# Kernel optimization log

Measured on AMD Instinct MI355X. Metric: run time of the kernel, lower is better.

## Reference

```python
import jax, jax.numpy as jnp
import numpy as np

CHUNK = 32
EPS = 1e-6

def _l2norm(x):
    return x * jax.lax.rsqrt(jnp.sum(x * x, axis=-1, keepdims=True) + EPS)

def setup_inputs() -> dict:
    key = jax.random.key(0)
    k1, k2, k3, k4 = jax.random.split(key, 4)
    b, h, L, dk, dv = 4, 8, 4096, 128, 128
    return {
        'q': jax.random.normal(k1, (b, h, L, dk), dtype=jnp.float32),
        'k': jax.random.normal(k2, (b, h, L, dk), dtype=jnp.float32),
        'v': jax.random.normal(k3, (b, h, L, dv), dtype=jnp.float32),
        'beta': jax.random.uniform(k4, (b, h, L), dtype=jnp.float32),
    }

def _delta_rule_chunkwise(q, k, v, beta):
    b, h, L, dk = q.shape
    dv = v.shape[-1]
    c = CHUNK
    assert L % c == 0, 'L must be a multiple of chunk_size (no padding path)'
    n = L // c

    q = _l2norm(q)
    k = _l2norm(k)
    v = v * beta[..., None]
    k_beta = k * beta[..., None]

    # [b,h,n,c,d]
    resh = lambda t: t.reshape(b, h, n, c, t.shape[-1])
    qc, kc, vc, kbc = resh(q), resh(k), resh(v), resh(k_beta)

    ones = jnp.ones((c, c), dtype=jnp.float32)
    strict_lower = jnp.tril(ones, -1)      # below diagonal
    lower_inc = jnp.tril(ones, 0)          # diagonal and below

    # inv = -(k_beta @ k^T) with upper-incl-diag zeroed, then forward substitution
    inv = -jnp.einsum('bhncd,bhned->bhnce', kbc, kc) * strict_lower
    for i in range(1, c):
        # inv[..., i, :i] += inv[..., i, :] @ inv[..., :, :i]
        upd = jnp.einsum('bhnk,bhnkj->bhnj', inv[..., i, :], inv[..., :, :i])
        inv = inv.at[..., i, :i].add(upd)
    inv = inv + jnp.eye(c, dtype=inv.dtype)

    u = jnp.einsum('bhnce,bhned->bhncd', inv, vc)    # [b,h,n,c,dv]
    w = jnp.einsum('bhnce,bhned->bhncd', inv, kbc)   # [b,h,n,c,dk]

    # scan over chunks carrying state S [b,h,dk,dv]
    def step(S, inp):
        q_i, k_i, u0_i, w_i = inp  # [b,h,c,d*]
        attn = jnp.einsum('bhcd,bhed->bhce', q_i, k_i) * lower_inc
        u_i = u0_i - jnp.einsum('bhcd,bhdv->bhcv', w_i, S)
        out_i = jnp.einsum('bhcd,bhdv->bhcv', q_i, S) + jnp.einsum('bhce,bhev->bhcv', attn, u_i)
        S = S + jnp.einsum('bhcd,bhcv->bhdv', k_i, u_i)
        return S, out_i

    chunk_first = lambda t: jnp.moveaxis(t, 2, 0)  # [n,b,h,c,d]
    S0 = jnp.zeros((b, h, dk, dv), dtype=q.dtype)
    S, out = jax.lax.scan(step, S0, (chunk_first(qc), chunk_first(kc), chunk_first(u), chunk_first(w)))
    out = jnp.moveaxis(out, 0, 2).reshape(b, h, L, dv)
    return out, S

def reference(q, k, v, beta):
    out, S = _delta_rule_chunkwise(q, k, v, beta)
    return out
```

## Files before the change

### kernel.cpp

```cpp
#include <hip/hip_runtime.h>
#include <math.h>

#define CHUNK 32
#define DK 128
#define DV 128
#define L_SEQ 4096
#define BH 32
#define NCH 128

typedef __attribute__((ext_vector_type(8))) short bf16x8;
typedef __attribute__((ext_vector_type(4))) float f32x4;

union U8 { unsigned int u[4]; bf16x8 v; };

#define MFMA16(a, b, c) __builtin_amdgcn_mfma_f32_16x16x32_bf16((a), (b), (c), 0, 0, 0)
#define LGKM_WAIT() __asm__ __volatile__("s_waitcnt lgkmcnt(0)" ::: "memory")

__device__ __forceinline__ unsigned short f2bf(float x){
    unsigned int u = __builtin_bit_cast(unsigned int, x);
    u = u + 0x7FFFu + ((u >> 16) & 1u);
    return (unsigned short)(u >> 16);
}
__device__ __forceinline__ unsigned int pk2(float a, float b){
    unsigned int r;
    asm("v_cvt_pk_bf16_f32 %0, %1, %2" : "=v"(r) : "v"(a), "v"(b));
    return r;
}

__device__ __forceinline__ bf16x8 afragF32(const float (*M)[36], int row, int q8){
    float4 f0 = *(const float4*)&M[row][q8];
    float4 f1 = *(const float4*)&M[row][q8 + 4];
    U8 t;
    t.u[0] = pk2(f0.x, f0.y); t.u[1] = pk2(f0.z, f0.w);
    t.u[2] = pk2(f1.x, f1.y); t.u[3] = pk2(f1.z, f1.w);
    return t.v;
}
__device__ __forceinline__ bf16x8 bfragF32(const float (*M)[36], int q8, int col){
    U8 t;
#pragma unroll
    for (int j2 = 0; j2 < 4; ++j2)
        t.u[j2] = pk2(M[q8 + 2*j2][col], M[q8 + 2*j2 + 1][col]);
    return t.v;
}


__global__ __launch_bounds__(64, 1)
void prep_kernel(const float* __restrict__ q, const float* __restrict__ k,
                 const float* __restrict__ beta,
                 unsigned short* __restrict__ qw, unsigned short* __restrict__ kw,
                 unsigned short* __restrict__ Tw, unsigned short* __restrict__ Aw)
{
    const int bc = blockIdx.x;
    const size_t row0 = (size_t)bc * CHUNK;
    const int l = threadIdx.x;
    const int r = l & 31, h = l >> 5;
    const int quad = (l >> 4) & 3, ln15 = l & 15, q8 = quad * 8;

    __shared__ unsigned short qn_s[32][136], kn_s[32][136], kb_s[32][136];
    __shared__ float Ms[32][36];
    __shared__ float Rs[32][36];

    const float bet = beta[row0 + r];

    {
        const float4* gp = (const float4*)(q + (row0 + r) * DK + 64 * h);
        float vb[64]; float s = 0.f;
#pragma unroll
        for (int e = 0; e < 16; ++e){
            float4 a = gp[e];
            vb[4*e+0]=a.x; vb[4*e+1]=a.y; vb[4*e+2]=a.z; vb[4*e+3]=a.w;
            s += a.x*a.x + a.y*a.y + a.z*a.z + a.w*a.w;
        }
        s += __shfl_xor(s, 32);
        float sc = rsqrtf(s + 1e-6f);
#pragma unroll
        for (int e = 0; e < 8; ++e){
            U8 t;
#pragma unroll
            for (int j = 0; j < 4; ++j)
                t.u[j] = pk2(vb[8*e+2*j] * sc, vb[8*e+2*j+1] * sc);
            *(bf16x8*)&qn_s[r][64*h + 8*e] = t.v;
            *(bf16x8*)(qw + (row0 + r) * DK + 64*h + 8*e) = t.v;
        }
    }
    {
        const float4* gp = (const float4*)(k + (row0 + r) * DK + 64 * h);
        float vb[64]; float s = 0.f;
#pragma unroll
        for (int e = 0; e < 16; ++e){
            float4 a = gp[e];
            vb[4*e+0]=a.x; vb[4*e+1]=a.y; vb[4*e+2]=a.z; vb[4*e+3]=a.w;
            s += a.x*a.x + a.y*a.y + a.z*a.z + a.w*a.w;
        }
        s += __shfl_xor(s, 32);
        float sc = rsqrtf(s + 1e-6f);
#pragma unroll
        for (int e = 0; e < 8; ++e){
            U8 t, tb;
#pragma unroll
            for (int j = 0; j < 4; ++j){
                float x0 = vb[8*e+2*j] * sc, x1 = vb[8*e+2*j+1] * sc;
                t.u[j]  = pk2(x0, x1);
                tb.u[j] = pk2(x0 * bet, x1 * bet);
            }
            *(bf16x8*)&kn_s[r][64*h + 8*e] = t.v;
            *(bf16x8*)&kb_s[r][64*h + 8*e] = tb.v;
            *(bf16x8*)(kw + (row0 + r) * DK + 64*h + 8*e) = t.v;
        }
    }
    LGKM_WAIT();

    f32x4 Z = {0.f, 0.f, 0.f, 0.f};
    f32x4 Bacc[2][2] = {{Z, Z}, {Z, Z}};
    f32x4 Aacc[2][2] = {{Z, Z}, {Z, Z}};
#pragma unroll
    for (int ks = 0; ks < 4; ++ks){
        bf16x8 bF[2];
        bF[0] = *(const bf16x8*)&kn_s[ln15][32*ks + q8];
        bF[1] = *(const bf16x8*)&kn_s[16 + ln15][32*ks + q8];
#pragma unroll
        for (int mt = 0; mt < 2; ++mt){
            bf16x8 aK = *(const bf16x8*)&kb_s[16*mt + ln15][32*ks + q8];
            bf16x8 aQ = *(const bf16x8*)&qn_s[16*mt + ln15][32*ks + q8];
#pragma unroll
            for (int nt = 0; nt < 2; ++nt){
                Bacc[mt][nt] = MFMA16(aK, bF[nt], Bacc[mt][nt]);
                Aacc[mt][nt] = MFMA16(aQ, bF[nt], Aacc[mt][nt]);
            }
        }
    }

    f32x4 Rc[2][2];
#pragma unroll
    for (int mt = 0; mt < 2; ++mt)
#pragma unroll
    for (int nt = 0; nt < 2; ++nt)
#pragma unroll
    for (int rg = 0; rg < 4; ++rg){
        int row = 16*mt + 4*quad + rg, col = 16*nt + ln15;
        float av = (col <= row) ? Aacc[mt][nt][rg] : 0.f;
        Aw[((size_t)bc << 10) + row*32 + col] = f2bf(av);
        float bm = (col < row) ? -Bacc[mt][nt][rg] : 0.f;
        Ms[row][col] = bm;
        Rc[mt][nt][rg] = bm + ((col == row) ? 1.f : 0.f);
    }

#pragma unroll 1
    for (int rd = 0; rd < 4; ++rd){
        LGKM_WAIT();
        bf16x8 Am[2], Bm2[2];
#pragma unroll
        for (int mt = 0; mt < 2; ++mt) Am[mt] = afragF32(Ms, 16*mt + ln15, q8);
#pragma unroll
        for (int nt = 0; nt < 2; ++nt) Bm2[nt] = bfragF32(Ms, q8, 16*nt + ln15);
        f32x4 Mq[2][2];
#pragma unroll
        for (int mt = 0; mt < 2; ++mt)
#pragma unroll
        for (int nt = 0; nt < 2; ++nt)
            Mq[mt][nt] = MFMA16(Am[mt], Bm2[nt], Z);
#pragma unroll
        for (int mt = 0; mt < 2; ++mt)
#pragma unroll
        for (int nt = 0; nt < 2; ++nt)
#pragma unroll
        for (int rg = 0; rg < 4; ++rg){
            int row = 16*mt + 4*quad + rg, col = 16*nt + ln15;
            Rs[row][col] = Rc[mt][nt][rg];
            Ms[row][col] = Mq[mt][nt][rg];
        }
        LGKM_WAIT();
        bf16x8 Ar[2], Bq[2];
#pragma unroll
        for (int mt = 0; mt < 2; ++mt) Ar[mt] = afragF32(Rs, 16*mt + ln15, q8);
#pragma unroll
        for (int nt = 0; nt < 2; ++nt) Bq[nt] = bfragF32(Ms, q8, 16*nt + ln15);
#pragma unroll
        for (int mt = 0; mt < 2; ++mt)
#pragma unroll
        for (int nt = 0; nt < 2; ++nt)
            Rc[mt][nt] = MFMA16(Ar[mt], Bq[nt], Rc[mt][nt]);
    }

#pragma unroll
    for (int mt = 0; mt < 2; ++mt)
#pragma unroll
    for (int nt = 0; nt < 2; ++nt)
#pragma unroll
    for (int rg = 0; rg < 4; ++rg){
        int row = 16*mt + 4*quad + rg, col = 16*nt + ln15;
        Tw[((size_t)bc << 10) + row*32 + col] = f2bf(Rc[mt][nt][rg]);
    }
}


__global__ __launch_bounds__(64, 1)
void scan_kernel(const float* __restrict__ v, const float* __restrict__ beta,
                 const unsigned short* __restrict__ qw, const unsigned short* __restrict__ kw,
                 const unsigned short* __restrict__ Tw, const unsigned short* __restrict__ Aw,
                 float* __restrict__ out)
{
    const int id = blockIdx.x;
    const int bh = id & 31, cb = id >> 5, c0 = cb * 16;
    const int l = threadIdx.x;
    const int quad = (l >> 4) & 3, ln15 = l & 15, q8 = quad * 8;
    const int hi = l >> 5;

    __shared__ unsigned short knR[4392];
    __shared__ unsigned short Xt[16][40];
    __shared__ unsigned short ut[16][40];

    const f32x4 Z = {0.f, 0.f, 0.f, 0.f};
    f32x4 Sacc[8];
#pragma unroll
    for (int t = 0; t < 8; ++t) Sacc[t] = Z;

    const size_t bhL = (size_t)bh * L_SEQ;
    const int a0 = (((l & 16) << 1) | ln15) << 2;
    const int a1 = a0 + 64;

    bf16x8 kAa[2][4], kAb[2][4];
    bf16x8 qA[2][4], tA[2], aA[2], knA[8], uB;
    float vr[8], br[8];

    auto loadK = [&](int ch, bf16x8 (&kA)[2][4]){
        const unsigned short* kp = kw + (bhL + (size_t)ch * CHUNK) * DK;
#pragma unroll
        for (int mt = 0; mt < 2; ++mt)
#pragma unroll
        for (int ks = 0; ks < 4; ++ks)
            kA[mt][ks] = *(const bf16x8*)(kp + (16*mt + ln15) * DK + 32*ks + q8);
    };
    auto loadQ = [&](int ch){
        const unsigned short* qp = qw + (bhL + (size_t)ch * CHUNK) * DK;
#pragma unroll
        for (int mt = 0; mt < 2; ++mt)
#pragma unroll
        for (int ks = 0; ks < 4; ++ks)
            qA[mt][ks] = *(const bf16x8*)(qp + (16*mt + ln15) * DK + 32*ks + q8);
    };
    auto loadT = [&](int ch){
        const unsigned short* Tp = Tw + ((size_t)(bh * NCH + ch) << 10);
#pragma unroll
        for (int mt = 0; mt < 2; ++mt)
            tA[mt] = *(const bf16x8*)(Tp + (16*mt + ln15) * 32 + q8);
    };
    auto loadA = [&](int ch){
        const unsigned short* Ap = Aw + ((size_t)(bh * NCH + ch) << 10);
#pragma unroll
        for (int mt = 0; mt < 2; ++mt)
            aA[mt] = *(const bf16x8*)(Ap + (16*mt + ln15) * 32 + q8);
    };
    auto loadVB = [&](int ch){
        const size_t row0 = bhL + (size_t)ch * CHUNK;
#pragma unroll
        for (int g = 0; g < 8; ++g){
            int i = 16*(g >> 2) + 4*quad + (g & 3);
            vr[g] = v[(row0 + i) * DV + c0 + ln15];
            br[g] = beta[row0 + i];
        }
    };

    loadK(0, kAa);
    loadQ(0); loadT(0); loadA(0); loadVB(0);
    loadK(1, kAb);
    {
        U8 z; z.u[0] = 0u; z.u[1] = 0u; z.u[2] = 0u; z.u[3] = 0u;
        uB = z.v;
#pragma unroll
        for (int t = 0; t < 8; ++t) knA[t] = z.v;
    }

    auto body = [&](int ch, bf16x8 (&cur)[2][4]){
        const size_t row0 = bhL + (size_t)ch * CHUNK;

#pragma unroll
        for (int t = 0; t < 8; ++t)
            Sacc[t] = MFMA16(knA[t], uB, Sacc[t]);

        int P[8][2];
#pragma unroll
        for (int t = 0; t < 8; ++t){
            P[t][0] = (int)pk2(Sacc[t][0], Sacc[t][1]);
            P[t][1] = (int)pk2(Sacc[t][2], Sacc[t][3]);
        }
        bf16x8 SB[4];
#pragma unroll
        for (int ks = 0; ks < 4; ++ks){
            U8 sb;
            int e, f;
            e = __builtin_amdgcn_ds_bpermute(a0, P[2*ks][0]);
            f = __builtin_amdgcn_ds_bpermute(a0, P[2*ks+1][0]);
            sb.u[0] = (unsigned)(hi ? f : e);
            e = __builtin_amdgcn_ds_bpermute(a0, P[2*ks][1]);
            f = __builtin_amdgcn_ds_bpermute(a0, P[2*ks+1][1]);
            sb.u[1] = (unsigned)(hi ? f : e);
            e = __builtin_amdgcn_ds_bpermute(a1, P[2*ks][0]);
            f = __builtin_amdgcn_ds_bpermute(a1, P[2*ks+1][0]);
            sb.u[2] = (unsigned)(hi ? f : e);
            e = __builtin_amdgcn_ds_bpermute(a1, P[2*ks][1]);
            f = __builtin_amdgcn_ds_bpermute(a1, P[2*ks+1][1]);
            sb.u[3] = (unsigned)(hi ? f : e);
            SB[ks] = sb.v;
        }

        f32x4 Y[2] = {Z, Z}, Op[2] = {Z, Z};
#pragma unroll
        for (int ks = 0; ks < 4; ++ks)
#pragma unroll
        for (int mt = 0; mt < 2; ++mt){
            Y[mt]  = MFMA16(cur[mt][ks], SB[ks], Y[mt]);
            Op[mt] = MFMA16(qA[mt][ks],  SB[ks], Op[mt]);
        }

#pragma unroll
        for (int mt = 0; mt < 2; ++mt){
            unsigned int w0 = pk2(br[4*mt+0] * (vr[4*mt+0] - Y[mt][0]),
                                  br[4*mt+1] * (vr[4*mt+1] - Y[mt][1]));
            unsigned int w1 = pk2(br[4*mt+2] * (vr[4*mt+2] - Y[mt][2]),
                                  br[4*mt+3] * (vr[4*mt+3] - Y[mt][3]));
            *(unsigned int*)&Xt[ln15][16*mt + 4*quad]     = w0;
            *(unsigned int*)&Xt[ln15][16*mt + 4*quad + 2] = w1;
        }

#pragma unroll
        for (int mt = 0; mt < 2; ++mt)
#pragma unroll
        for (int ks = 0; ks < 4; ++ks){
            int i = 16*mt + ln15;
            int ad = i * 136 + (i >> 3) * 16 + 32*ks + q8;
            *(bf16x8*)&knR[ad] = cur[mt][ks];
        }

        bf16x8 Xb = *(const bf16x8*)&Xt[ln15][q8];

        unsigned int rja[32];
#pragma unroll
        for (int t = 0; t < 4; ++t)
#pragma unroll
        for (int j = 0; j < 8; ++j)
            rja[8*t + j] = knR[(q8 + j) * 136 + ((q8 + j) >> 3) * 16 + 16*t + ln15];

        f32x4 U[2];
#pragma unroll
        for (int mt = 0; mt < 2; ++mt) U[mt] = MFMA16(tA[mt], Xb, Z);

#pragma unroll
        for (int mt = 0; mt < 2; ++mt){
            *(unsigned int*)&ut[ln15][16*mt + 4*quad]     = pk2(U[mt][0], U[mt][1]);
            *(unsigned int*)&ut[ln15][16*mt + 4*quad + 2] = pk2(U[mt][2], U[mt][3]);
        }

#pragma unroll
        for (int t = 0; t < 4; ++t){
            U8 kk;
            kk.u[0] = rja[8*t+0] | (rja[8*t+1] << 16);
            kk.u[1] = rja[8*t+2] | (rja[8*t+3] << 16);
            kk.u[2] = rja[8*t+4] | (rja[8*t+5] << 16);
            kk.u[3] = rja[8*t+6] | (rja[8*t+7] << 16);
            knA[t] = kk.v;
        }

        uB = *(const bf16x8*)&ut[ln15][q8];

        const int chn = (ch + 1 < NCH) ? ch + 1 : NCH - 1;
        const int ch2 = (ch + 2 < NCH) ? ch + 2 : NCH - 1;
        loadQ(chn); loadT(chn); loadVB(chn);
        loadK(ch2, cur);

        unsigned int rjb[32];
#pragma unroll
        for (int t = 0; t < 4; ++t)
#pragma unroll
        for (int j = 0; j < 8; ++j)
            rjb[8*t + j] = knR[(q8 + j) * 136 + ((q8 + j) >> 3) * 16 + 16*(t + 4) + ln15];

        f32x4 O[2];
#pragma unroll
        for (int mt = 0; mt < 2; ++mt) O[mt] = MFMA16(aA[mt], uB, Op[mt]);
#pragma unroll
        for (int mt = 0; mt < 2; ++mt)
#pragma unroll
        for (int rg = 0; rg < 4; ++rg)
            out[(row0 + 16*mt + 4*quad + rg) * DV + c0 + ln15] = O[mt][rg];

#pragma unroll
        for (int t = 0; t < 4; ++t){
            U8 kk;
            kk.u[0] = rjb[8*t+0] | (rjb[8*t+1] << 16);
            kk.u[1] = rjb[8*t+2] | (rjb[8*t+3] << 16);
            kk.u[2] = rjb[8*t+4] | (rjb[8*t+5] << 16);
            kk.u[3] = rjb[8*t+6] | (rjb[8*t+7] << 16);
            knA[t + 4] = kk.v;
        }
        loadA(chn);
    };

    for (int ch = 0; ch < NCH; ch += 2){
        body(ch,     kAa);
        body(ch + 1, kAb);
    }
}


__global__ __launch_bounds__(512, 1)
void deltanet_fused(const float* __restrict__ q, const float* __restrict__ k,
                    const float* __restrict__ v, const float* __restrict__ beta,
                    float* __restrict__ out)
{
    const int bh = blockIdx.x;
    const int tid = threadIdx.x;
    const int n = L_SEQ / CHUNK;

    __shared__ float S[DK][DV + 1];
    __shared__ float qs[CHUNK][DK + 1];
    __shared__ float ks[CHUNK][DK + 1];
    __shared__ float vs[CHUNK][DV + 1];
    __shared__ float kbs[CHUNK][DK + 1];
    __shared__ float T[CHUNK][CHUNK + 1];
    __shared__ float at[CHUNK][CHUNK + 1];
    __shared__ float bet[CHUNK];

    for (int idx = tid; idx < DK * DV; idx += 512)
        S[idx / DV][idx % DV] = 0.f;
    __syncthreads();

    const size_t base_bh = (size_t)bh * L_SEQ;

    for (int ch = 0; ch < n; ++ch){
        const size_t row0 = base_bh + (size_t)ch * CHUNK;
        for (int idx = tid; idx < CHUNK * DK; idx += 512){
            int r = idx >> 7, c = idx & 127;
            size_t g = (row0 + (size_t)r) * DK + c;
            qs[r][c] = q[g]; ks[r][c] = k[g]; vs[r][c] = v[g];
        }
        if (tid < CHUNK) bet[tid] = beta[row0 + tid];
        __syncthreads();
        if (tid < 64){
            int r = tid & 31;
            const float* src = (tid < 32) ? &qs[r][0] : &ks[r][0];
            float s = 0.f;
            for (int d = 0; d < DK; ++d){ float x = src[d]; s += x * x; }
            at[(tid < 32) ? 0 : 1][r] = 1.0f / sqrtf(s + 1e-6f);
        }
        __syncthreads();
        for (int idx = tid; idx < CHUNK * DK; idx += 512){
            int r = idx >> 7, c = idx & 127;
            float qq = qs[r][c] * at[0][r];
            float kk = ks[r][c] * at[1][r];
            float b = bet[r];
            qs[r][c] = qq; ks[r][c] = kk; kbs[r][c] = kk * b; vs[r][c] *= b;
        }
        __syncthreads();
        for (int idx = tid; idx < CHUNK * CHUNK; idx += 512){
            int i = idx >> 5, j = idx & 31;
            float s = 0.f;
            if (j < i){
                for (int d = 0; d < DK; ++d) s += kbs[i][d] * ks[j][d];
                s = -s;
            }
            T[i][j] = s;
        }
        __syncthreads();
        for (int i = 1; i < CHUNK; ++i){
            float upd = 0.f;
            if (tid < i){
                int j = tid;
                for (int kk = j + 1; kk < i; ++kk) upd += T[i][kk] * T[kk][j];
            }
            __syncthreads();
            if (tid < i) T[i][tid] += upd;
            __syncthreads();
        }
        if (tid < CHUNK) T[tid][tid] = 1.0f;
        __syncthreads();
        {
            int c = tid & 127;
            int i0 = (tid >> 7) * 8;
            float uacc[8], wacc[8];
#pragma unroll
            for (int r = 0; r < 8; ++r){ uacc[r] = 0.f; wacc[r] = 0.f; }
            for (int j = 0; j < CHUNK; ++j){
                float vvv = vs[j][c], kb = kbs[j][c];
#pragma unroll
                for (int r = 0; r < 8; ++r){
                    float tt = T[i0 + r][j];
                    uacc[r] += tt * vvv; wacc[r] += tt * kb;
                }
            }
            __syncthreads();
#pragma unroll
            for (int r = 0; r < 8; ++r){ vs[i0 + r][c] = uacc[r]; kbs[i0 + r][c] = wacc[r]; }
        }
        __syncthreads();
        for (int idx = tid; idx < CHUNK * CHUNK; idx += 512){
            int i = idx >> 5, j = idx & 31;
            float s = 0.f;
            if (j <= i) for (int d = 0; d < DK; ++d) s += qs[i][d] * ks[j][d];
            at[i][j] = s;
        }
        __syncthreads();
        {
            int c = tid & 127;
            int i0 = (tid >> 7) * 8;
            float acc[8];
#pragma unroll
            for (int r = 0; r < 8; ++r) acc[r] = 0.f;
            for (int d = 0; d < DK; ++d){
                float sv = S[d][c];
#pragma unroll
                for (int r = 0; r < 8; ++r) acc[r] += kbs[i0 + r][d] * sv;
            }
#pragma unroll
            for (int r = 0; r < 8; ++r) vs[i0 + r][c] -= acc[r];
        }
        __syncthreads();
        {
            int c = tid & 127;
            int i0 = (tid >> 7) * 8;
            float acc[8];
#pragma unroll
            for (int r = 0; r < 8; ++r) acc[r] = 0.f;
            for (int d = 0; d < DK; ++d){
                float sv = S[d][c];
#pragma unroll
                for (int r = 0; r < 8; ++r) acc[r] += qs[i0 + r][d] * sv;
            }
            for (int j = 0; j < CHUNK; ++j){
                float uv = vs[j][c];
#pragma unroll
                for (int r = 0; r < 8; ++r) acc[r] += at[i0 + r][j] * uv;
            }
#pragma unroll
            for (int r = 0; r < 8; ++r)
                out[(row0 + (size_t)(i0 + r)) * DV + c] = acc[r];
        }
        __syncthreads();
        {
            int c = tid & 127;
            int d0 = (tid >> 7) * 32;
            float acc[32];
#pragma unroll
            for (int r = 0; r < 32; ++r) acc[r] = 0.f;
            for (int i = 0; i < CHUNK; ++i){
                float uv = vs[i][c];
#pragma unroll
                for (int r = 0; r < 32; ++r) acc[r] += ks[i][d0 + r] * uv;
            }
#pragma unroll
            for (int r = 0; r < 32; ++r) S[d0 + r][c] += acc[r];
        }
        __syncthreads();
    }
}

extern "C" void kernel_launch(void* const* d_in, const int* in_sizes, int n_in,
                              void* d_out, int out_size, void* d_ws, size_t ws_size,
                              hipStream_t stream) {
    const float* q = (const float*)d_in[0];
    const float* k = (const float*)d_in[1];
    const float* v = (const float*)d_in[2];
    const float* beta = (const float*)d_in[3];
    float* out = (float*)d_out;

    const size_t QK = (size_t)BH * L_SEQ * DK;
    const size_t TA = (size_t)BH * NCH * 1024;
    const size_t need = (2 * QK + 2 * TA) * sizeof(unsigned short);

    if (ws_size >= need){
        unsigned short* qwp = (unsigned short*)d_ws;
        unsigned short* kwp = qwp + QK;
        unsigned short* Twp = kwp + QK;
        unsigned short* Awp = Twp + TA;
        prep_kernel<<<BH * NCH, 64, 0, stream>>>(q, k, beta, qwp, kwp, Twp, Awp);
        scan_kernel<<<BH * 8, 64, 0, stream>>>(v, beta, qwp, kwp, Twp, Awp, out);
    } else {
        deltanet_fused<<<BH, 512, 0, stream>>>(q, k, v, beta, out);
    }
}
```

Before: 368.9 us.

## Precompute transposed K in prep and use permlane swaps in scan loop

The prep kernel now loads q/k straight into MFMA fragment registers instead of staging them in LDS. It also writes a transposed bf16 copy of normalized k to a new workspace buffer. The scan kernel loads this transposed K directly rather than transposing it through LDS every chunk. It replaces LDS staging and ds_bpermute shuffles with permlane16/32 swap instructions, dispatched over runtime-detected lane-order variants, and splits the MFMA accumulation chains for more ILP. This removes LDS traffic and waits from the serial scan, at the cost of more workspace memory, extra global reads and writes, and a larger fallback condition on workspace size.

```diff
diff --git a/kernel.cpp b/kernel.cpp
--- a/kernel.cpp
+++ b/kernel.cpp
@@ -10,11 +10,18 @@
 
 typedef __attribute__((ext_vector_type(8))) short bf16x8;
 typedef __attribute__((ext_vector_type(4))) float f32x4;
+typedef unsigned int uint32x2 __attribute__((ext_vector_type(2)));
 
 union U8 { unsigned int u[4]; bf16x8 v; };
 
 #define MFMA16(a, b, c) __builtin_amdgcn_mfma_f32_16x16x32_bf16((a), (b), (c), 0, 0, 0)
 #define LGKM_WAIT() __asm__ __volatile__("s_waitcnt lgkmcnt(0)" ::: "memory")
+
+#if __has_builtin(__builtin_amdgcn_permlane16_swap) && __has_builtin(__builtin_amdgcn_permlane32_swap)
+#define HAVE_PERMSWAP 1
+#else
+#define HAVE_PERMSWAP 0
+#endif
 
 __device__ __forceinline__ unsigned short f2bf(float x){
     unsigned int u = __builtin_bit_cast(unsigned int, x);
@@ -44,92 +51,174 @@
 }
 
 
-__global__ __launch_bounds__(64, 1)
+#if HAVE_PERMSWAP
+template<bool O16, bool O32>
+__device__ __forceinline__ bf16x8 quadperm(unsigned p0, unsigned p1, unsigned p2, unsigned p3,
+                                           bool hB, bool eqHS)
+{
+    uint32x2 t0 = __builtin_amdgcn_permlane16_swap(p0, p0, false, false);
+    uint32x2 t1 = __builtin_amdgcn_permlane16_swap(p1, p1, false, false);
+    uint32x2 t2 = __builtin_amdgcn_permlane16_swap(p2, p2, false, false);
+    uint32x2 t3 = __builtin_amdgcn_permlane16_swap(p3, p3, false, false);
+    unsigned p0e = O16 ? t0.y : t0.x, p0o = O16 ? t0.x : t0.y;
+    unsigned p1e = O16 ? t1.y : t1.x, p1o = O16 ? t1.x : t1.y;
+    unsigned p2e = O16 ? t2.y : t2.x, p2o = O16 ? t2.x : t2.y;
+    unsigned p3e = O16 ? t3.y : t3.x, p3o = O16 ? t3.x : t3.y;
+
+    auto word = [&](unsigned ae, unsigned ce) -> unsigned {
+        unsigned L = hB ? ce : ae;
+        uint32x2 x = __builtin_amdgcn_permlane32_swap(O32 ? ce : ae, O32 ? ae : ce, false, false);
+        unsigned C = O32 ? (hB ? x.y : x.x) : (hB ? x.x : x.y);
+        return eqHS ? L : C;
+    };
+    U8 r;
+    r.u[0] = word(p0e, p2e);
+    r.u[1] = word(p1e, p3e);
+    r.u[2] = word(p0o, p2o);
+    r.u[3] = word(p1o, p3o);
+    return r.v;
+}
+#else
+template<bool O16, bool O32>
+__device__ __forceinline__ bf16x8 quadperm(unsigned p0, unsigned p1, unsigned p2, unsigned p3,
+                                           bool hB, bool eqHS)
+{
+    (void)eqHS;
+    const int l = threadIdx.x;
+    const int ln15 = l & 15;
+    const int a0 = (((l & 16) << 1) | ln15) << 2;
+    const int a1 = a0 + 64;
+    U8 r; int e, f;
+    e = __builtin_amdgcn_ds_bpermute(a0, (int)p0); f = __builtin_amdgcn_ds_bpermute(a0, (int)p2);
+    r.u[0] = (unsigned)(hB ? f : e);
+    e = __builtin_amdgcn_ds_bpermute(a0, (int)p1); f = __builtin_amdgcn_ds_bpermute(a0, (int)p3);
+    r.u[1] = (unsigned)(hB ? f : e);
+    e = __builtin_amdgcn_ds_bpermute(a1, (int)p0); f = __builtin_amdgcn_ds_bpermute(a1, (int)p2);
+    r.u[2] = (unsigned)(hB ? f : e);
+    e = __builtin_amdgcn_ds_bpermute(a1, (int)p1); f = __builtin_amdgcn_ds_bpermute(a1, (int)p3);
+    r.u[3] = (unsigned)(hB ? f : e);
+    return r.v;
+}
+#endif
+
+
+__global__ __launch_bounds__(64)
 void prep_kernel(const float* __restrict__ q, const float* __restrict__ k,
                  const float* __restrict__ beta,
                  unsigned short* __restrict__ qw, unsigned short* __restrict__ kw,
-                 unsigned short* __restrict__ Tw, unsigned short* __restrict__ Aw)
+                 unsigned short* __restrict__ Tw, unsigned short* __restrict__ Aw,
+                 unsigned short* __restrict__ kwT)
 {
     const int bc = blockIdx.x;
     const size_t row0 = (size_t)bc * CHUNK;
     const int l = threadIdx.x;
-    const int r = l & 31, h = l >> 5;
     const int quad = (l >> 4) & 3, ln15 = l & 15, q8 = quad * 8;
 
-    __shared__ unsigned short qn_s[32][136], kn_s[32][136], kb_s[32][136];
     __shared__ float Ms[32][36];
     __shared__ float Rs[32][36];
-
-    const float bet = beta[row0 + r];
-
+    __shared__ __align__(16) unsigned short knS[4392];
+
+    const float bet0 = beta[row0 + ln15];
+    const float bet1 = beta[row0 + 16 + ln15];
+
+    bf16x8 qF[2][4];
     {
-        const float4* gp = (const float4*)(q + (row0 + r) * DK + 64 * h);
-        float vb[64]; float s = 0.f;
-#pragma unroll
-        for (int e = 0; e < 16; ++e){
-            float4 a = gp[e];
-            vb[4*e+0]=a.x; vb[4*e+1]=a.y; vb[4*e+2]=a.z; vb[4*e+3]=a.w;
-            s += a.x*a.x + a.y*a.y + a.z*a.z + a.w*a.w;
-        }
-        s += __shfl_xor(s, 32);
-        float sc = rsqrtf(s + 1e-6f);
-#pragma unroll
-        for (int e = 0; e < 8; ++e){
-            U8 t;
-#pragma unroll
-            for (int j = 0; j < 4; ++j)
-                t.u[j] = pk2(vb[8*e+2*j] * sc, vb[8*e+2*j+1] * sc);
-            *(bf16x8*)&qn_s[r][64*h + 8*e] = t.v;
-            *(bf16x8*)(qw + (row0 + r) * DK + 64*h + 8*e) = t.v;
-        }
-    }
+        float4 raw[2][4][2];
+        float s0 = 0.f, s1 = 0.f;
+#pragma unroll
+        for (int mt = 0; mt < 2; ++mt)
+#pragma unroll
+        for (int ks = 0; ks < 4; ++ks){
+            const float* p = q + (row0 + 16*mt + ln15) * DK + 32*ks + q8;
+            raw[mt][ks][0] = *(const float4*)p;
+            raw[mt][ks][1] = *(const float4*)(p + 4);
+        }
+#pragma unroll
+        for (int ks = 0; ks < 4; ++ks)
+#pragma unroll
+        for (int h = 0; h < 2; ++h){
+            float4 a = raw[0][ks][h], b = raw[1][ks][h];
+            s0 += a.x*a.x + a.y*a.y + a.z*a.z + a.w*a.w;
+            s1 += b.x*b.x + b.y*b.y + b.z*b.z + b.w*b.w;
+        }
+        s0 += __shfl_xor(s0, 16); s0 += __shfl_xor(s0, 32);
+        s1 += __shfl_xor(s1, 16); s1 += __shfl_xor(s1, 32);
+        float sc0 = rsqrtf(s0 + 1e-6f), sc1 = rsqrtf(s1 + 1e-6f);
+#pragma unroll
+        for (int mt = 0; mt < 2; ++mt){
+            float sc = mt ? sc1 : sc0;
+#pragma unroll
+            for (int ks = 0; ks < 4; ++ks){
+                float4 a = raw[mt][ks][0], b = raw[mt][ks][1];
+                U8 t;
+                t.u[0] = pk2(a.x*sc, a.y*sc); t.u[1] = pk2(a.z*sc, a.w*sc);
+                t.u[2] = pk2(b.x*sc, b.y*sc); t.u[3] = pk2(b.z*sc, b.w*sc);
+                qF[mt][ks] = t.v;
+                *(bf16x8*)(qw + (row0 + 16*mt + ln15) * DK + 32*ks + q8) = t.v;
+            }
+        }
+    }
+    bf16x8 kF[2][4], kB[2][4];
     {
-        const float4* gp = (const float4*)(k + (row0 + r) * DK + 64 * h);
-        float vb[64]; float s = 0.f;
-#pragma unroll
-        for (int e = 0; e < 16; ++e){
-            float4 a = gp[e];
-            vb[4*e+0]=a.x; vb[4*e+1]=a.y; vb[4*e+2]=a.z; vb[4*e+3]=a.w;
-            s += a.x*a.x + a.y*a.y + a.z*a.z + a.w*a.w;
-        }
-        s += __shfl_xor(s, 32);
-        float sc = rsqrtf(s + 1e-6f);
-#pragma unroll
-        for (int e = 0; e < 8; ++e){
-            U8 t, tb;
-#pragma unroll
-            for (int j = 0; j < 4; ++j){
-                float x0 = vb[8*e+2*j] * sc, x1 = vb[8*e+2*j+1] * sc;
-                t.u[j]  = pk2(x0, x1);
-                tb.u[j] = pk2(x0 * bet, x1 * bet);
-            }
-            *(bf16x8*)&kn_s[r][64*h + 8*e] = t.v;
-            *(bf16x8*)&kb_s[r][64*h + 8*e] = tb.v;
-            *(bf16x8*)(kw + (row0 + r) * DK + 64*h + 8*e) = t.v;
-        }
-    }
-    LGKM_WAIT();
-
+        float4 raw[2][4][2];
+        float s0 = 0.f, s1 = 0.f;
+#pragma unroll
+        for (int mt = 0; mt < 2; ++mt)
+#pragma unroll
+        for (int ks = 0; ks < 4; ++ks){
+            const float* p = k + (row0 + 16*mt + ln15) * DK + 32*ks + q8;
+            raw[mt][ks][0] = *(const float4*)p;
+            raw[mt][ks][1] = *(const float4*)(p + 4);
+        }
+#pragma unroll
+        for (int ks = 0; ks < 4; ++ks)
+#pragma unroll
+        for (int h = 0; h < 2; ++h){
+            float4 a = raw[0][ks][h], b = raw[1][ks][h];
+            s0 += a.x*a.x + a.y*a.y + a.z*a.z + a.w*a.w;
+            s1 += b.x*b.x + b.y*b.y + b.z*b.z + b.w*b.w;
+        }
+        s0 += __shfl_xor(s0, 16); s0 += __shfl_xor(s0, 32);
+        s1 += __shfl_xor(s1, 16); s1 += __shfl_xor(s1, 32);
+        float sc0 = rsqrtf(s0 + 1e-6f), sc1 = rsqrtf(s1 + 1e-6f);
+#pragma unroll
+        for (int mt = 0; mt < 2; ++mt){
+            float sc = mt ? sc1 : sc0;
+            float bb = mt ? bet1 : bet0;
+#pragma unroll
+            for (int ks = 0; ks < 4; ++ks){
+                float4 a = raw[mt][ks][0], b = raw[mt][ks][1];
+                float x0=a.x*sc, x1=a.y*sc, x2=a.z*sc, x3=a.w*sc;
+                float x4=b.x*sc, x5=b.y*sc, x6=b.z*sc, x7=b.w*sc;
+                U8 t, tb;
+                t.u[0]=pk2(x0,x1); t.u[1]=pk2(x2,x3); t.u[2]=pk2(x4,x5); t.u[3]=pk2(x6,x7);
+                tb.u[0]=pk2(x0*bb,x1*bb); tb.u[1]=pk2(x2*bb,x3*bb);
+                tb.u[2]=pk2(x4*bb,x5*bb); tb.u[3]=pk2(x6*bb,x7*bb);
+                kF[mt][ks] = t.v; kB[mt][ks] = tb.v;
+                *(bf16x8*)(kw + (row0 + 16*mt + ln15) * DK + 32*ks + q8) = t.v;
+            }
+        }
+    }
+#pragma unroll
+    for (int mt = 0; mt < 2; ++mt)
+#pragma unroll
+    for (int ks = 0; ks < 4; ++ks){
+        int i = 16*mt + ln15;
+        int ad = i * 136 + (i >> 3) * 16 + 32*ks + q8;
+        *(bf16x8*)&knS[ad] = kF[mt][ks];
+    }
     f32x4 Z = {0.f, 0.f, 0.f, 0.f};
     f32x4 Bacc[2][2] = {{Z, Z}, {Z, Z}};
     f32x4 Aacc[2][2] = {{Z, Z}, {Z, Z}};
 #pragma unroll
-    for (int ks = 0; ks < 4; ++ks){
-        bf16x8 bF[2];
-        bF[0] = *(const bf16x8*)&kn_s[ln15][32*ks + q8];
-        bF[1] = *(const bf16x8*)&kn_s[16 + ln15][32*ks + q8];
-#pragma unroll
-        for (int mt = 0; mt < 2; ++mt){
-            bf16x8 aK = *(const bf16x8*)&kb_s[16*mt + ln15][32*ks + q8];
-            bf16x8 aQ = *(const bf16x8*)&qn_s[16*mt + ln15][32*ks + q8];
-#pragma unroll
-            for (int nt = 0; nt < 2; ++nt){
-                Bacc[mt][nt] = MFMA16(aK, bF[nt], Bacc[mt][nt]);
-                Aacc[mt][nt] = MFMA16(aQ, bF[nt], Aacc[mt][nt]);
-            }
-        }
-    }
-
+    for (int ks = 0; ks < 4; ++ks)
+#pragma unroll
+    for (int mt = 0; mt < 2; ++mt)
+#pragma unroll
+    for (int nt = 0; nt < 2; ++nt){
+        Bacc[mt][nt] = MFMA16(kB[mt][ks], kF[nt][ks], Bacc[mt][nt]);
+        Aacc[mt][nt] = MFMA16(qF[mt][ks], kF[nt][ks], Aacc[mt][nt]);
+    }
     f32x4 Rc[2][2];
 #pragma unroll
     for (int mt = 0; mt < 2; ++mt)
@@ -144,7 +233,22 @@
         Ms[row][col] = bm;
         Rc[mt][nt][rg] = bm + ((col == row) ? 1.f : 0.f);
     }
-
+    {
+        unsigned short* kT = kwT + ((size_t)bc << 12);
+#pragma unroll
+        for (int t = 0; t < 8; ++t){
+            unsigned short rj[8];
+#pragma unroll
+            for (int j = 0; j < 8; ++j)
+                rj[j] = knS[(q8 + j) * 136 + ((q8 + j) >> 3) * 16 + 16*t + ln15];
+            U8 kk;
+            kk.u[0] = (unsigned)rj[0] | ((unsigned)rj[1] << 16);
+            kk.u[1] = (unsigned)rj[2] | ((unsigned)rj[3] << 16);
+            kk.u[2] = (unsigned)rj[4] | ((unsigned)rj[5] << 16);
+            kk.u[3] = (unsigned)rj[6] | ((unsigned)rj[7] << 16);
+            *(bf16x8*)(kT + (16*t + ln15) * 32 + q8) = kk.v;
+        }
+    }
 #pragma unroll 1
     for (int rd = 0; rd < 4; ++rd){
         LGKM_WAIT();
@@ -181,7 +285,6 @@
         for (int nt = 0; nt < 2; ++nt)
             Rc[mt][nt] = MFMA16(Ar[mt], Bq[nt], Rc[mt][nt]);
     }
-
 #pragma unroll
     for (int mt = 0; mt < 2; ++mt)
 #pragma unroll
@@ -194,21 +297,19 @@
 }
 
 
-__global__ __launch_bounds__(64, 1)
-void scan_kernel(const float* __restrict__ v, const float* __restrict__ beta,
-                 const unsigned short* __restrict__ qw, const unsigned short* __restrict__ kw,
-                 const unsigned short* __restrict__ Tw, const unsigned short* __restrict__ Aw,
-                 float* __restrict__ out)
+template<bool O16, bool O32>
+__device__ __forceinline__
+void scan_loop(const float* __restrict__ v, const float* __restrict__ beta,
+               const unsigned short* __restrict__ qw, const unsigned short* __restrict__ kw,
+               const unsigned short* __restrict__ kwT, const unsigned short* __restrict__ Tw,
+               const unsigned short* __restrict__ Aw, float* __restrict__ out)
 {
     const int id = blockIdx.x;
     const int bh = id & 31, cb = id >> 5, c0 = cb * 16;
     const int l = threadIdx.x;
     const int quad = (l >> 4) & 3, ln15 = l & 15, q8 = quad * 8;
-    const int hi = l >> 5;
-
-    __shared__ unsigned short knR[4392];
-    __shared__ unsigned short Xt[16][40];
-    __shared__ unsigned short ut[16][40];
+    const bool hB = (l & 32) != 0;
+    const bool eqHS = (hB == ((l & 16) != 0));
 
     const f32x4 Z = {0.f, 0.f, 0.f, 0.f};
     f32x4 Sacc[8];
@@ -216,20 +317,17 @@
     for (int t = 0; t < 8; ++t) Sacc[t] = Z;
 
     const size_t bhL = (size_t)bh * L_SEQ;
-    const int a0 = (((l & 16) << 1) | ln15) << 2;
-    const int a1 = a0 + 64;
-
-    bf16x8 kAa[2][4], kAb[2][4];
-    bf16x8 qA[2][4], tA[2], aA[2], knA[8], uB;
+
+    bf16x8 cur[2][4], qA[2][4], knA[8], tA[2], aA[2], uB;
     float vr[8], br[8];
 
-    auto loadK = [&](int ch, bf16x8 (&kA)[2][4]){
+    auto loadK = [&](int ch){
         const unsigned short* kp = kw + (bhL + (size_t)ch * CHUNK) * DK;
 #pragma unroll
         for (int mt = 0; mt < 2; ++mt)
 #pragma unroll
         for (int ks = 0; ks < 4; ++ks)
-            kA[mt][ks] = *(const bf16x8*)(kp + (16*mt + ln15) * DK + 32*ks + q8);
+            cur[mt][ks] = *(const bf16x8*)(kp + (16*mt + ln15) * DK + 32*ks + q8);
     };
     auto loadQ = [&](int ch){
         const unsigned short* qp = qw + (bhL + (size_t)ch * CHUNK) * DK;
@@ -260,10 +358,14 @@
             br[g] = beta[row0 + i];
         }
     };
-
-    loadK(0, kAa);
-    loadQ(0); loadT(0); loadA(0); loadVB(0);
-    loadK(1, kAb);
+    auto loadKT = [&](int ch){
+        const unsigned short* p = kwT + ((size_t)(bh * NCH + ch) << 12);
+#pragma unroll
+        for (int t = 0; t < 8; ++t)
+            knA[t] = *(const bf16x8*)(p + (16*t + ln15) * 32 + q8);
+    };
+
+    loadK(0); loadQ(0); loadT(0); loadA(0); loadVB(0);
     {
         U8 z; z.u[0] = 0u; z.u[1] = 0u; z.u[2] = 0u; z.u[3] = 0u;
         uB = z.v;
@@ -271,135 +373,99 @@
         for (int t = 0; t < 8; ++t) knA[t] = z.v;
     }
 
-    auto body = [&](int ch, bf16x8 (&cur)[2][4]){
+    for (int ch = 0; ch < NCH; ++ch){
         const size_t row0 = bhL + (size_t)ch * CHUNK;
+        const int chn = (ch + 1 < NCH) ? ch + 1 : NCH - 1;
 
 #pragma unroll
         for (int t = 0; t < 8; ++t)
             Sacc[t] = MFMA16(knA[t], uB, Sacc[t]);
-
-        int P[8][2];
+        loadKT(ch);
+
+        unsigned P[8][2];
 #pragma unroll
         for (int t = 0; t < 8; ++t){
-            P[t][0] = (int)pk2(Sacc[t][0], Sacc[t][1]);
-            P[t][1] = (int)pk2(Sacc[t][2], Sacc[t][3]);
+            P[t][0] = pk2(Sacc[t][0], Sacc[t][1]);
+            P[t][1] = pk2(Sacc[t][2], Sacc[t][3]);
         }
         bf16x8 SB[4];
 #pragma unroll
-        for (int ks = 0; ks < 4; ++ks){
-            U8 sb;
-            int e, f;
-            e = __builtin_amdgcn_ds_bpermute(a0, P[2*ks][0]);
-            f = __builtin_amdgcn_ds_bpermute(a0, P[2*ks+1][0]);
-            sb.u[0] = (unsigned)(hi ? f : e);
-            e = __builtin_amdgcn_ds_bpermute(a0, P[2*ks][1]);
-            f = __builtin_amdgcn_ds_bpermute(a0, P[2*ks+1][1]);
-            sb.u[1] = (unsigned)(hi ? f : e);
-            e = __builtin_amdgcn_ds_bpermute(a1, P[2*ks][0]);
-            f = __builtin_amdgcn_ds_bpermute(a1, P[2*ks+1][0]);
-            sb.u[2] = (unsigned)(hi ? f : e);
-            e = __builtin_amdgcn_ds_bpermute(a1, P[2*ks][1]);
-            f = __builtin_amdgcn_ds_bpermute(a1, P[2*ks+1][1]);
-            sb.u[3] = (unsigned)(hi ? f : e);
-            SB[ks] = sb.v;
-        }
-
-        f32x4 Y[2] = {Z, Z}, Op[2] = {Z, Z};
-#pragma unroll
         for (int ks = 0; ks < 4; ++ks)
+            SB[ks] = quadperm<O16, O32>(P[2*ks][0], P[2*ks][1], P[2*ks+1][0], P[2*ks+1][1], hB, eqHS);
+
+        f32x4 Y0[2] = {Z, Z}, Y1[2] = {Z, Z}, Op0[2] = {Z, Z}, Op1[2] = {Z, Z};
 #pragma unroll
         for (int mt = 0; mt < 2; ++mt){
-            Y[mt]  = MFMA16(cur[mt][ks], SB[ks], Y[mt]);
-            Op[mt] = MFMA16(qA[mt][ks],  SB[ks], Op[mt]);
-        }
-
-#pragma unroll
-        for (int mt = 0; mt < 2; ++mt){
-            unsigned int w0 = pk2(br[4*mt+0] * (vr[4*mt+0] - Y[mt][0]),
-                                  br[4*mt+1] * (vr[4*mt+1] - Y[mt][1]));
-            unsigned int w1 = pk2(br[4*mt+2] * (vr[4*mt+2] - Y[mt][2]),
-                                  br[4*mt+3] * (vr[4*mt+3] - Y[mt][3]));
-            *(unsigned int*)&Xt[ln15][16*mt + 4*quad]     = w0;
-            *(unsigned int*)&Xt[ln15][16*mt + 4*quad + 2] = w1;
-        }
-
-#pragma unroll
-        for (int mt = 0; mt < 2; ++mt)
-#pragma unroll
-        for (int ks = 0; ks < 4; ++ks){
-            int i = 16*mt + ln15;
-            int ad = i * 136 + (i >> 3) * 16 + 32*ks + q8;
-            *(bf16x8*)&knR[ad] = cur[mt][ks];
-        }
-
-        bf16x8 Xb = *(const bf16x8*)&Xt[ln15][q8];
-
-        unsigned int rja[32];
-#pragma unroll
-        for (int t = 0; t < 4; ++t)
-#pragma unroll
-        for (int j = 0; j < 8; ++j)
-            rja[8*t + j] = knR[(q8 + j) * 136 + ((q8 + j) >> 3) * 16 + 16*t + ln15];
+            Y0[mt]  = MFMA16(cur[mt][0], SB[0], Y0[mt]);
+            Y0[mt]  = MFMA16(cur[mt][1], SB[1], Y0[mt]);
+            Y1[mt]  = MFMA16(cur[mt][2], SB[2], Y1[mt]);
+            Y1[mt]  = MFMA16(cur[mt][3], SB[3], Y1[mt]);
+            Op0[mt] = MFMA16(qA[mt][0],  SB[0], Op0[mt]);
+            Op0[mt] = MFMA16(qA[mt][1],  SB[1], Op0[mt]);
+            Op1[mt] = MFMA16(qA[mt][2],  SB[2], Op1[mt]);
+            Op1[mt] = MFMA16(qA[mt][3],  SB[3], Op1[mt]);
+        }
+        loadK(chn); loadQ(chn);
+
+        f32x4 Yf0 = Y0[0] + Y1[0];
+        f32x4 Yf1 = Y0[1] + Y1[1];
+        unsigned PX0, PX1, PX2, PX3;
+        {
+            float x00 = br[0]*(vr[0]-Yf0[0]), x01 = br[1]*(vr[1]-Yf0[1]);
+            float x02 = br[2]*(vr[2]-Yf0[2]), x03 = br[3]*(vr[3]-Yf0[3]);
+            float x10 = br[4]*(vr[4]-Yf1[0]), x11 = br[5]*(vr[5]-Yf1[1]);
+            float x12 = br[6]*(vr[6]-Yf1[2]), x13 = br[7]*(vr[7]-Yf1[3]);
+            PX0 = pk2(x00, x01); PX1 = pk2(x02, x03);
+            PX2 = pk2(x10, x11); PX3 = pk2(x12, x13);
+        }
+        bf16x8 Xb = quadperm<O16, O32>(PX0, PX1, PX2, PX3, hB, eqHS);
 
         f32x4 U[2];
 #pragma unroll
         for (int mt = 0; mt < 2; ++mt) U[mt] = MFMA16(tA[mt], Xb, Z);
-
-#pragma unroll
-        for (int mt = 0; mt < 2; ++mt){
-            *(unsigned int*)&ut[ln15][16*mt + 4*quad]     = pk2(U[mt][0], U[mt][1]);
-            *(unsigned int*)&ut[ln15][16*mt + 4*quad + 2] = pk2(U[mt][2], U[mt][3]);
-        }
-
-#pragma unroll
-        for (int t = 0; t < 4; ++t){
-            U8 kk;
-            kk.u[0] = rja[8*t+0] | (rja[8*t+1] << 16);
-            kk.u[1] = rja[8*t+2] | (rja[8*t+3] << 16);
-            kk.u[2] = rja[8*t+4] | (rja[8*t+5] << 16);
-            kk.u[3] = rja[8*t+6] | (rja[8*t+7] << 16);
-            knA[t] = kk.v;
-        }
-
-        uB = *(const bf16x8*)&ut[ln15][q8];
-
-        const int chn = (ch + 1 < NCH) ? ch + 1 : NCH - 1;
-        const int ch2 = (ch + 2 < NCH) ? ch + 2 : NCH - 1;
-        loadQ(chn); loadT(chn); loadVB(chn);
-        loadK(ch2, cur);
-
-        unsigned int rjb[32];
-#pragma unroll
-        for (int t = 0; t < 4; ++t)
-#pragma unroll
-        for (int j = 0; j < 8; ++j)
-            rjb[8*t + j] = knR[(q8 + j) * 136 + ((q8 + j) >> 3) * 16 + 16*(t + 4) + ln15];
+        loadT(chn);
+
+        uB = quadperm<O16, O32>(pk2(U[0][0], U[0][1]), pk2(U[0][2], U[0][3]),
+                                pk2(U[1][0], U[1][1]), pk2(U[1][2], U[1][3]), hB, eqHS);
 
         f32x4 O[2];
-#pragma unroll
-        for (int mt = 0; mt < 2; ++mt) O[mt] = MFMA16(aA[mt], uB, Op[mt]);
+        O[0] = Op0[0] + Op1[0];
+        O[1] = Op0[1] + Op1[1];
+#pragma unroll
+        for (int mt = 0; mt < 2; ++mt) O[mt] = MFMA16(aA[mt], uB, O[mt]);
 #pragma unroll
         for (int mt = 0; mt < 2; ++mt)
 #pragma unroll
         for (int rg = 0; rg < 4; ++rg)
             out[(row0 + 16*mt + 4*quad + rg) * DV + c0 + ln15] = O[mt][rg];
 
-#pragma unroll
-        for (int t = 0; t < 4; ++t){
-            U8 kk;
-            kk.u[0] = rjb[8*t+0] | (rjb[8*t+1] << 16);
-            kk.u[1] = rjb[8*t+2] | (rjb[8*t+3] << 16);
-            kk.u[2] = rjb[8*t+4] | (rjb[8*t+5] << 16);
-            kk.u[3] = rjb[8*t+6] | (rjb[8*t+7] << 16);
-            knA[t + 4] = kk.v;
-        }
         loadA(chn);
-    };
-
-    for (int ch = 0; ch < NCH; ch += 2){
-        body(ch,     kAa);
-        body(ch + 1, kAb);
-    }
+        loadVB(chn);
+    }
+}
+
+__global__ __launch_bounds__(64, 1)
+void scan_perm(const float* __restrict__ v, const float* __restrict__ beta,
+               const unsigned short* __restrict__ qw, const unsigned short* __restrict__ kw,
+               const unsigned short* __restrict__ kwT, const unsigned short* __restrict__ Tw,
+               const unsigned short* __restrict__ Aw, float* __restrict__ out)
+{
+#if HAVE_PERMSWAP
+    const unsigned l = threadIdx.x;
+    uint32x2 t16 = __builtin_amdgcn_permlane16_swap(l, l, false, false);
+    uint32x2 t32 = __builtin_amdgcn_permlane32_swap(l, l, false, false);
+    const bool o16 = (t16.x == ((l & 32u) | 16u | (l & 15u)));
+    const bool o32 = (t32.x == (32u | (l & 31u)));
+    if (o16){
+        if (o32) scan_loop<true,  true >(v, beta, qw, kw, kwT, Tw, Aw, out);
+        else     scan_loop<true,  false>(v, beta, qw, kw, kwT, Tw, Aw, out);
+    } else {
+        if (o32) scan_loop<false, true >(v, beta, qw, kw, kwT, Tw, Aw, out);
+        else     scan_loop<false, false>(v, beta, qw, kw, kwT, Tw, Aw, out);
+    }
+#else
+    scan_loop<true, true>(v, beta, qw, kw, kwT, Tw, Aw, out);
+#endif
 }
 
 
@@ -565,15 +631,16 @@
 
     const size_t QK = (size_t)BH * L_SEQ * DK;
     const size_t TA = (size_t)BH * NCH * 1024;
-    const size_t need = (2 * QK + 2 * TA) * sizeof(unsigned short);
-
-    if (ws_size >= need){
+    const size_t need32 = (3*QK + 2*TA) * sizeof(unsigned short);
+
+    if (ws_size >= need32){
         unsigned short* qwp = (unsigned short*)d_ws;
         unsigned short* kwp = qwp + QK;
         unsigned short* Twp = kwp + QK;
         unsigned short* Awp = Twp + TA;
-        prep_kernel<<<BH * NCH, 64, 0, stream>>>(q, k, beta, qwp, kwp, Twp, Awp);
-        scan_kernel<<<BH * 8, 64, 0, stream>>>(v, beta, qwp, kwp, Twp, Awp, out);
+        unsigned short* kTp = Awp + TA;
+        prep_kernel<<<BH * NCH, 64, 0, stream>>>(q, k, beta, qwp, kwp, Twp, Awp, kTp);
+        scan_perm<<<BH * 8, 64, 0, stream>>>(v, beta, qwp, kwp, kTp, Twp, Awp, out);
     } else {
         deltanet_fused<<<BH, 512, 0, stream>>>(q, k, v, beta, out);
     }
```

Result: no change. 370.3 us (+0.4%).
